# Kernel tuning notes

Hardware: AMD Instinct MI355X
Metric: run time of the kernel (lower is better)

Reference implementation:

```python
import jax, jax.numpy as jnp
import numpy as np

B, T, DIM = 2, 2048, 2048
H, DH = 16, 128
QC, KVC = 512, 512
DD = 64  # decoupled rope dim


def _rope_freqs(t, dd, theta=10000.0):
    inv = 1.0 / (theta ** (np.arange(0, dd, 2, dtype=np.float32) / dd))  # [dd/2]
    ang = np.arange(t, dtype=np.float32)[:, None] * inv[None, :]         # [T, dd/2]
    return jnp.asarray(np.stack([np.cos(ang), np.sin(ang)], axis=-1))    # [T, dd/2, 2]


def setup_inputs() -> dict:
    key = jax.random.key(0)
    ks = jax.random.split(key, 10)
    def w(k, i, o):
        return jax.random.normal(k, (i, o), jnp.float32) / np.sqrt(i)
    x = jax.random.normal(ks[0], (B, T, DIM), jnp.float32)
    freqs_cis = _rope_freqs(T, DD)
    neg = jnp.float32(-1e9)
    mask = jnp.where(jnp.tril(jnp.ones((T, T), bool)), 0.0, neg).astype(jnp.float32)
    return {
        "x": x, "freqs_cis": freqs_cis, "mask": mask,
        "W_dq": w(ks[1], DIM, QC), "W_uq": w(ks[2], QC, H * DH),
        "W_dkv": w(ks[3], DIM, KVC), "W_uk": w(ks[4], KVC, H * DH),
        "W_uv": w(ks[5], KVC, H * DH), "W_qr": w(ks[6], QC, H * DD),
        "W_kr": w(ks[7], DIM, DD), "W_o": w(ks[8], H * DH, DIM),
    }


def _apply_rope(t, freqs_cis):
    # t: [B, T, H, DD]; freqs_cis: [T, DD/2, 2]
    tp = t.reshape(*t.shape[:-1], -1, 2)               # [B,T,H,DD/2,2]
    cos = freqs_cis[None, :, None, :, 0]
    sin = freqs_cis[None, :, None, :, 1]
    x1, x2 = tp[..., 0], tp[..., 1]
    rot = jnp.stack([x1 * cos - x2 * sin, x1 * sin + x2 * cos], axis=-1)
    return rot.reshape(t.shape)


def reference(x, freqs_cis, mask, W_dq, W_uq, W_dkv, W_uk, W_uv, W_qr, W_kr, W_o):
    q_c = x @ W_dq                                     # [B,T,QC]
    kv_c = x @ W_dkv                                   # [B,T,KVC]
    q_rope = (q_c @ W_qr).reshape(B, T, H, DD)
    kv_rope = jnp.broadcast_to((x @ W_kr)[:, :, None, :], (B, T, H, DD))
    q_rope = _apply_rope(q_rope, freqs_cis)
    kv_rope = _apply_rope(kv_rope, freqs_cis)
    q = (q_c @ W_uq).reshape(B, T, H, DH)
    k = (kv_c @ W_uk).reshape(B, T, H, DH)
    v = (kv_c @ W_uv).reshape(B, T, H, DH)
    q = jnp.concatenate([q, q_rope], axis=-1)          # [B,T,H,DH+DD]
    k = jnp.concatenate([k, kv_rope], axis=-1)
    scale = 1.0 / np.sqrt(DH + DD)
    scores = jnp.einsum("bqhd,bkhd->bhqk", q, k) * scale + mask[None, None]
    attn = jax.nn.softmax(scores, axis=-1)
    out = jnp.einsum("bhqk,bkhd->bqhd", attn, v).reshape(B, T, H * DH)
    return out @ W_o
```

## Files before the change

### kernel.cpp

```cpp
#include <hip/hip_runtime.h>
#include <hip/hip_bf16.h>
#include <cstdint>
#include <cstddef>

typedef __bf16 bf16_t;
typedef __attribute__((ext_vector_type(8))) __bf16 bf16x8;
typedef __attribute__((ext_vector_type(4))) __bf16 bf16x4;
typedef __attribute__((ext_vector_type(4))) float f32x4;

#define B_ 2
#define T_ 2048
#define DIM_ 2048
#define H_ 16
#define DH_ 128
#define DD_ 64
#define DQK_ 192
#define QSTRIDE_ 3072
#define BT_ 4096

__device__ __forceinline__ void gload16(const void* g, void* lds) {
  __builtin_amdgcn_global_load_lds(
      (const __attribute__((address_space(1))) unsigned int*)g,
      (__attribute__((address_space(3))) unsigned int*)lds, 16, 0, 0);
}

struct bf16_4 { bf16_t a, b, c, d; };
__global__ void cast_f32_bf16(const float* __restrict__ in, bf16_t* __restrict__ out, int n4) {
  int i = blockIdx.x * blockDim.x + threadIdx.x;
  if (i >= n4) return;
  float4 v = ((const float4*)in)[i];
  bf16_4 r{(bf16_t)v.x, (bf16_t)v.y, (bf16_t)v.z, (bf16_t)v.w};
  ((bf16_4*)out)[i] = r;
}

__global__ void transpose_cast(const float* __restrict__ W, bf16_t* __restrict__ Wt,
                               int K, int N, int Np) {
  __shared__ float tile[32][33];
  int k0 = blockIdx.x * 32, n0 = blockIdx.y * 32;
  int tx = threadIdx.x, ty = threadIdx.y;
#pragma unroll
  for (int i = 0; i < 4; ++i) {
    int k = k0 + ty + i * 8, n = n0 + tx;
    float v = (k < K && n < N) ? W[(size_t)k * N + n] : 0.f;
    tile[ty + i * 8][tx] = v;
  }
  __syncthreads();
#pragma unroll
  for (int i = 0; i < 4; ++i) {
    int n = n0 + ty + i * 8, k = k0 + tx;
    if (n < Np && k < K) Wt[(size_t)n * K + k] = (bf16_t)tile[tx][ty + i * 8];
  }
}

__global__ void transpose_v(const bf16_t* __restrict__ V, bf16_t* __restrict__ Vt) {
  __shared__ bf16_t tile[64 * 64];
  int id = blockIdx.x;
  int t0 = (id & 31) * 64;
  int d0 = ((id >> 5) & 1) * 64;
  int bh = id >> 6;
  int b = bh >> 4, h = bh & 15;
  int t = threadIdx.x;
#pragma unroll
  for (int it = 0; it < 2; ++it) {
    int idx = it * 256 + t;
    int tt = idx >> 3, c = idx & 7;
    bf16x8 v = *(const bf16x8*)&V[(size_t)(b * T_ + t0 + tt) * 2048 + h * 128 + d0 + c * 8];
    int sw = (tt ^ (tt >> 3)) & 7;
    *(bf16x8*)((char*)tile + tt * 128 + 16 * (c ^ sw)) = v;
  }
  __syncthreads();
#pragma unroll
  for (int it = 0; it < 2; ++it) {
    int idx = it * 256 + t;
    int dr = idx >> 3, c = idx & 7;
    bf16_t tmp[8];
#pragma unroll
    for (int u = 0; u < 8; ++u) {
      int sw = (u ^ c) & 7;
      tmp[u] = *(const bf16_t*)((const char*)tile + (8 * c + u) * 128 + ((2 * dr) ^ (16 * sw)));
    }
    *(bf16x8*)&Vt[((size_t)bh * 128 + d0 + dr) * T_ + t0 + c * 8] = *(bf16x8*)tmp;
  }
}

template <int MODE>
__global__ __launch_bounds__(256) void gemm_bt(const bf16_t* __restrict__ A,
                                               const bf16_t* __restrict__ Bt,
                                               void* __restrict__ C0v,
                                               void* __restrict__ C1v,
                                               void* __restrict__ C2v,
                                               int M, int N, int K, int ldc) {
  __shared__ bf16_t As[128 * 32];
  __shared__ bf16_t Bs[128 * 32];
  const int t = threadIdx.x;
  const int w = t >> 6, l = t & 63, l15 = l & 15, lhi = l >> 4;
  const int m0 = blockIdx.y * 128, n0 = blockIdx.x * 128;
  const int wr = (w >> 1) * 64, wc = (w & 1) * 64;

  f32x4 zero = {0.f, 0.f, 0.f, 0.f};
  f32x4 acc[4][4];
#pragma unroll
  for (int m = 0; m < 4; ++m)
#pragma unroll
    for (int n = 0; n < 4; ++n) acc[m][n] = zero;

  const int e0 = t * 8;
  const int r0 = e0 >> 5, c0 = e0 & 31;
  const int e1 = 2048 + t * 8;
  const int r1 = e1 >> 5, c1 = e1 & 31;

  for (int k0 = 0; k0 < K; k0 += 32) {
    gload16(A + (size_t)(m0 + r0) * K + k0 + c0, &As[e0]);
    gload16(A + (size_t)(m0 + r1) * K + k0 + c1, &As[e1]);
    gload16(Bt + (size_t)(n0 + r0) * K + k0 + c0, &Bs[e0]);
    gload16(Bt + (size_t)(n0 + r1) * K + k0 + c1, &Bs[e1]);
    __syncthreads();
    bf16x8 af[4], bfr[4];
#pragma unroll
    for (int m = 0; m < 4; ++m)
      af[m] = *(const bf16x8*)&As[(wr + m * 16 + l15) * 32 + lhi * 8];
#pragma unroll
    for (int n = 0; n < 4; ++n)
      bfr[n] = *(const bf16x8*)&Bs[(wc + n * 16 + l15) * 32 + lhi * 8];
#pragma unroll
    for (int m = 0; m < 4; ++m)
#pragma unroll
      for (int n = 0; n < 4; ++n)
        acc[m][n] = __builtin_amdgcn_mfma_f32_16x16x32_bf16(af[m], bfr[n], acc[m][n], 0, 0, 0);
    __syncthreads();
  }

#pragma unroll
  for (int m = 0; m < 4; ++m) {
#pragma unroll
    for (int n = 0; n < 4; ++n) {
#pragma unroll
      for (int r = 0; r < 4; ++r) {
        int row = m0 + wr + m * 16 + lhi * 4 + r;
        int col = n0 + wc + n * 16 + l15;
        float v = acc[m][n][r];
        if (MODE == 1) {
          ((float*)C0v)[(size_t)row * ldc + col] = v;
        } else if (MODE == 3) {
          if (col < 512)       ((bf16_t*)C0v)[(size_t)row * 512 + col] = (bf16_t)v;
          else if (col < 1024) ((bf16_t*)C1v)[(size_t)row * 512 + (col - 512)] = (bf16_t)v;
          else if (col < 1088) ((bf16_t*)C2v)[(size_t)row * 64 + (col - 1024)] = (bf16_t)v;
        } else if (MODE == 4) {
          if (col < 2048) ((bf16_t*)C0v)[(size_t)row * QSTRIDE_ + (col >> 7) * DQK_ + (col & 127)] = (bf16_t)v;
          else            ((bf16_t*)C1v)[(size_t)row * 1024 + (col - 2048)] = (bf16_t)v;
        } else if (MODE == 5) {
          if (col < 2048) ((bf16_t*)C0v)[(size_t)row * QSTRIDE_ + (col >> 7) * DQK_ + (col & 127)] = (bf16_t)v;
          else            ((bf16_t*)C1v)[(size_t)row * 2048 + (col - 2048)] = (bf16_t)v;
        }
      }
    }
  }
}

__global__ void rope_q(const bf16_t* __restrict__ qr, const float* __restrict__ fr,
                       bf16_t* __restrict__ Q) {
  int idx = blockIdx.x * 256 + threadIdx.x;
  int j = idx & 31;
  int h = (idx >> 5) & 15;
  int row = idx >> 9;
  int tt = row & (T_ - 1);
  float x1 = (float)qr[(size_t)row * 1024 + h * 64 + 2 * j];
  float x2 = (float)qr[(size_t)row * 1024 + h * 64 + 2 * j + 1];
  float c = fr[tt * 64 + 2 * j], s = fr[tt * 64 + 2 * j + 1];
  bf16_t o0 = (bf16_t)(x1 * c - x2 * s);
  bf16_t o1 = (bf16_t)(x1 * s + x2 * c);
  size_t o = (size_t)row * QSTRIDE_ + h * DQK_ + 128 + 2 * j;
  Q[o] = o0;
  Q[o + 1] = o1;
}

__global__ void rope_k(const bf16_t* __restrict__ kr, const float* __restrict__ fr,
                       bf16_t* __restrict__ Kb) {
  int idx = blockIdx.x * 256 + threadIdx.x;
  int j = idx & 31;
  int row = idx >> 5;
  int tt = row & (T_ - 1);
  float x1 = (float)kr[(size_t)row * 64 + 2 * j];
  float x2 = (float)kr[(size_t)row * 64 + 2 * j + 1];
  float c = fr[tt * 64 + 2 * j], s = fr[tt * 64 + 2 * j + 1];
  union { bf16_t h2[2]; unsigned u; } pk;
  pk.h2[0] = (bf16_t)(x1 * c - x2 * s);
  pk.h2[1] = (bf16_t)(x1 * s + x2 * c);
#pragma unroll
  for (int h = 0; h < H_; ++h) {
    *(unsigned*)&Kb[(size_t)row * QSTRIDE_ + h * DQK_ + 128 + 2 * j] = pk.u;
  }
}

#define KLDB 200
#define VLDB 72
#define PLDB 68

__global__ __launch_bounds__(256, 2) void flash_attn3(const bf16_t* __restrict__ Q,
                                                      const bf16_t* __restrict__ Kb,
                                                      const bf16_t* __restrict__ Vt,
                                                      bf16_t* __restrict__ Ob) {
  __shared__ bf16_t Ks[64 * KLDB];
  __shared__ bf16_t Vs[128 * VLDB];
  __shared__ bf16_t Ps[4][16 * PLDB];

  const int t = threadIdx.x, w = t >> 6, l = t & 63, l15 = l & 15, lhi = l >> 4;
  const int id = blockIdx.x;
  const int xcd = id & 7, sub = id >> 3;
  const int bh = xcd * 4 + (sub >> 4);
  const int qp = sub & 15;
  const int b = bh >> 4, h = bh & 15;
  const int qa = qp, qb = 31 - qp;
  const float scale = 0.07216878364870322f;

  int rK[6], cK[6];
#pragma unroll
  for (int i = 0; i < 6; ++i) { int idx = i * 256 + t; rK[i] = idx / 24; cK[i] = idx % 24; }
  const int rVt = t >> 3, cV = t & 7;
  const bf16_t* kbase = Kb + (size_t)b * T_ * QSTRIDE_ + h * DQK_;
  const bf16_t* vbase = Vt + (size_t)bh * DH_ * T_;

  bf16x8 kreg[6], vreg[4];
#define LOAD_TILE(K0)                                                                      \
  do {                                                                                     \
    _Pragma("unroll") for (int i = 0; i < 6; ++i)                                          \
        kreg[i] = *(const bf16x8*)(kbase + (size_t)((K0) + rK[i]) * QSTRIDE_ + cK[i] * 8); \
    _Pragma("unroll") for (int i = 0; i < 4; ++i)                                          \
        vreg[i] = *(const bf16x8*)(vbase + (size_t)(i * 32 + rVt) * T_ + (K0) + cV * 8);   \
  } while (0)
#define WRITE_TILE()                                                                       \
  do {                                                                                     \
    _Pragma("unroll") for (int i = 0; i < 6; ++i)                                          \
        *(bf16x8*)&Ks[rK[i] * KLDB + cK[i] * 8] = kreg[i];                                 \
    _Pragma("unroll") for (int i = 0; i < 4; ++i)                                          \
        *(bf16x8*)&Vs[(i * 32 + rVt) * VLDB + cV * 8] = vreg[i];                           \
  } while (0)

  f32x4 zero = {0.f, 0.f, 0.f, 0.f};

  LOAD_TILE(0);
  WRITE_TILE();
  __syncthreads();

  for (int pass = 0; pass < 2; ++pass) {
    const int qt = pass ? qb : qa;

    bf16x8 qf[6];
    {
      const bf16_t* qrow = Q + ((size_t)(b * T_ + qt * 64 + w * 16 + l15)) * QSTRIDE_ + h * DQK_;
#pragma unroll
      for (int kc = 0; kc < 6; ++kc) qf[kc] = *(const bf16x8*)(qrow + kc * 32 + lhi * 8);
    }

    float m_r[4], l_r[4];
    f32x4 accO[8];
#pragma unroll
    for (int r = 0; r < 4; ++r) { m_r[r] = -1e30f; l_r[r] = 0.f; }
#pragma unroll
    for (int n = 0; n < 8; ++n) accO[n] = zero;

    for (int kt = 0; kt <= qt; ++kt) {
      const bool last = (kt == qt);
      const bool haveNext = !(pass == 1 && last);
      if (haveNext) LOAD_TILE(last ? 0 : (kt + 1) * 64);

      f32x4 s[4];
#pragma unroll
      for (int n = 0; n < 4; ++n) s[n] = zero;
      __builtin_amdgcn_s_setprio(1);
#pragma unroll
      for (int kc = 0; kc < 6; ++kc) {
#pragma unroll
        for (int n = 0; n < 4; ++n) {
          bf16x8 kf = *(const bf16x8*)&Ks[(n * 16 + l15) * KLDB + kc * 32 + lhi * 8];
          s[n] = __builtin_amdgcn_mfma_f32_16x16x32_bf16(qf[kc], kf, s[n], 0, 0, 0);
        }
      }
      __builtin_amdgcn_s_setprio(0);

#pragma unroll
      for (int n = 0; n < 4; ++n)
#pragma unroll
        for (int r = 0; r < 4; ++r) {
          float v = s[n][r] * scale;
          if (last) {
            int qq = w * 16 + lhi * 4 + r;
            int kk = n * 16 + l15;
            if (kk > qq) v = -1e30f;
          }
          s[n][r] = v;
        }
      float mn[4], corr[4];
#pragma unroll
      for (int r = 0; r < 4; ++r) {
        float v = fmaxf(fmaxf(s[0][r], s[1][r]), fmaxf(s[2][r], s[3][r]));
#pragma unroll
        for (int off = 1; off < 16; off <<= 1) v = fmaxf(v, __shfl_xor(v, off, 64));
        mn[r] = fmaxf(m_r[r], v);
        corr[r] = __expf(m_r[r] - mn[r]);
        m_r[r] = mn[r];
      }
      float rs[4] = {0.f, 0.f, 0.f, 0.f};
#pragma unroll
      for (int n = 0; n < 4; ++n)
#pragma unroll
        for (int r = 0; r < 4; ++r) {
          float p = __expf(s[n][r] - mn[r]);
          rs[r] += p;
          Ps[w][(lhi * 4 + r) * PLDB + n * 16 + l15] = (bf16_t)p;
        }
#pragma unroll
      for (int r = 0; r < 4; ++r) {
        float v = rs[r];
#pragma unroll
        for (int off = 1; off < 16; off <<= 1) v += __shfl_xor(v, off, 64);
        l_r[r] = l_r[r] * corr[r] + v;
      }
#pragma unroll
      for (int n = 0; n < 8; ++n)
#pragma unroll
        for (int r = 0; r < 4; ++r) accO[n][r] *= corr[r];

      __builtin_amdgcn_s_setprio(1);
#pragma unroll
      for (int kc = 0; kc < 2; ++kc) {
        bf16x4 p0 = *(const bf16x4*)&Ps[w][l15 * PLDB + kc * 32 + lhi * 8];
        bf16x4 p1 = *(const bf16x4*)&Ps[w][l15 * PLDB + kc * 32 + lhi * 8 + 4];
        bf16x8 pf = __builtin_shufflevector(p0, p1, 0, 1, 2, 3, 4, 5, 6, 7);
#pragma unroll
        for (int n = 0; n < 8; ++n) {
          bf16x8 vf = *(const bf16x8*)&Vs[(n * 16 + l15) * VLDB + kc * 32 + lhi * 8];
          accO[n] = __builtin_amdgcn_mfma_f32_16x16x32_bf16(pf, vf, accO[n], 0, 0, 0);
        }
      }
      __builtin_amdgcn_s_setprio(0);

      __syncthreads();
      if (haveNext) WRITE_TILE();
      __syncthreads();
    }

    {
      float inv[4];
#pragma unroll
      for (int r = 0; r < 4; ++r) inv[r] = 1.0f / l_r[r];
#pragma unroll
      for (int n = 0; n < 8; ++n)
#pragma unroll
        for (int r = 0; r < 4; ++r) {
          size_t row = (size_t)(b * T_ + qt * 64 + w * 16 + lhi * 4 + r);
          Ob[row * (H_ * DH_) + h * DH_ + n * 16 + l15] = (bf16_t)(accO[n][r] * inv[r]);
        }
    }
  }
#undef LOAD_TILE
#undef WRITE_TILE
}

extern "C" void kernel_launch(void* const* d_in, const int* in_sizes, int n_in,
                              void* d_out, int out_size, void* d_ws, size_t ws_size,
                              hipStream_t stream) {
  (void)in_sizes; (void)n_in; (void)out_size; (void)ws_size;
  const float* x    = (const float*)d_in[0];
  const float* fr   = (const float*)d_in[1];
  const float* Wdq  = (const float*)d_in[3];
  const float* Wuq  = (const float*)d_in[4];
  const float* Wdkv = (const float*)d_in[5];
  const float* Wuk  = (const float*)d_in[6];
  const float* Wuv  = (const float*)d_in[7];
  const float* Wqr  = (const float*)d_in[8];
  const float* Wkr  = (const float*)d_in[9];
  const float* Wo   = (const float*)d_in[10];
  float* out = (float*)d_out;

  char* ws = (char*)d_ws;
  size_t off = 0;
  auto alloc = [&](size_t bytes) -> void* {
    void* p = ws + off;
    off += (bytes + 255) & ~(size_t)255;
    return p;
  };
  bf16_t* x_bf   = (bf16_t*)alloc((size_t)BT_ * DIM_ * 2);
  bf16_t* Bt1    = (bf16_t*)alloc((size_t)1152 * 2048 * 2);
  bf16_t* Bt2    = (bf16_t*)alloc((size_t)3072 * 512 * 2);
  bf16_t* Bt3    = (bf16_t*)alloc((size_t)4096 * 512 * 2);
  bf16_t* Wo_t   = (bf16_t*)alloc((size_t)2048 * 2048 * 2);
  bf16_t* q_c    = (bf16_t*)alloc((size_t)BT_ * 512 * 2);
  bf16_t* kv_c   = (bf16_t*)alloc((size_t)BT_ * 512 * 2);
  bf16_t* q_rb   = (bf16_t*)alloc((size_t)BT_ * 1024 * 2);
  bf16_t* k_rb   = (bf16_t*)alloc((size_t)BT_ * 64 * 2);
  bf16_t* Qbuf   = (bf16_t*)alloc((size_t)BT_ * QSTRIDE_ * 2);
  bf16_t* Kbuf   = (bf16_t*)alloc((size_t)BT_ * QSTRIDE_ * 2);
  bf16_t* Vbuf   = (bf16_t*)alloc((size_t)BT_ * 2048 * 2);
  bf16_t* Vt_g   = (bf16_t*)alloc((size_t)BT_ * 2048 * 2);
  bf16_t* AObuf  = (bf16_t*)alloc((size_t)BT_ * 2048 * 2);

  dim3 tb(32, 8);
  cast_f32_bf16<<<(BT_ * DIM_ / 4 + 255) / 256, 256, 0, stream>>>(x, x_bf, BT_ * DIM_ / 4);
  transpose_cast<<<dim3(64, 16), tb, 0, stream>>>(Wdq,  Bt1,                        2048, 512, 512);
  transpose_cast<<<dim3(64, 16), tb, 0, stream>>>(Wdkv, Bt1 + (size_t)512 * 2048,   2048, 512, 512);
  transpose_cast<<<dim3(64, 4),  tb, 0, stream>>>(Wkr,  Bt1 + (size_t)1024 * 2048,  2048, 64, 128);
  transpose_cast<<<dim3(16, 64), tb, 0, stream>>>(Wuq,  Bt2,                        512, 2048, 2048);
  transpose_cast<<<dim3(16, 32), tb, 0, stream>>>(Wqr,  Bt2 + (size_t)2048 * 512,   512, 1024, 1024);
  transpose_cast<<<dim3(16, 64), tb, 0, stream>>>(Wuk,  Bt3,                        512, 2048, 2048);
  transpose_cast<<<dim3(16, 64), tb, 0, stream>>>(Wuv,  Bt3 + (size_t)2048 * 512,   512, 2048, 2048);
  transpose_cast<<<dim3(64, 64), tb, 0, stream>>>(Wo,   Wo_t,                       2048, 2048, 2048);

  gemm_bt<3><<<dim3(9, 32),  256, 0, stream>>>(x_bf, Bt1, q_c, kv_c, k_rb, BT_, 1088, 2048, 0);
  gemm_bt<4><<<dim3(24, 32), 256, 0, stream>>>(q_c,  Bt2, Qbuf, q_rb, nullptr, BT_, 3072, 512, 0);
  gemm_bt<5><<<dim3(32, 32), 256, 0, stream>>>(kv_c, Bt3, Kbuf, Vbuf, nullptr, BT_, 4096, 512, 0);

  transpose_v<<<2048, 256, 0, stream>>>(Vbuf, Vt_g);

  rope_q<<<(BT_ * H_ * 32) / 256, 256, 0, stream>>>(q_rb, fr, Qbuf);
  rope_k<<<(BT_ * 32) / 256, 256, 0, stream>>>(k_rb, fr, Kbuf);

  flash_attn3<<<512, 256, 0, stream>>>(Qbuf, Kbuf, Vt_g, AObuf);

  gemm_bt<1><<<dim3(16, 32), 256, 0, stream>>>(AObuf, Wo_t, out, nullptr, nullptr, BT_, 2048, 2048, 2048);
}
```

Before: 324.3 us.

## Rewrite flash attention with 128-row Q tiles, double-buffered async LDS loads and swizzle

The attention kernel now handles 128 query rows per block, with each wave owning 32 rows across two MFMA sub-tiles that share each K/V fragment read from LDS. K/V tiles are staged with direct global-to-LDS loads into double buffers using an XOR swizzle instead of padded rows, and the second barrier per step is removed. Grid shrinks to 256 blocks with one block per CU and causal pairing across 16 tiles. The intent is better reuse of LDS data and overlap of loads with compute. The cost is fewer waves for latency hiding, and waves on the diagonal tiles idle while others finish.

```diff
diff --git a/kernel.cpp b/kernel.cpp
--- a/kernel.cpp
+++ b/kernel.cpp
@@ -192,169 +192,200 @@
   }
 }
 
-#define KLDB 200
-#define VLDB 72
+#define KSLOT 24
+#define KBYTES (64 * KSLOT * 16)
+#define VSLOT 8
+#define VBYTES (128 * VSLOT * 16)
 #define PLDB 68
-
-__global__ __launch_bounds__(256, 2) void flash_attn3(const bf16_t* __restrict__ Q,
+#define PSBYTES (4 * 32 * PLDB * 2)
+#define SMEM_TOTAL (2 * KBYTES + 2 * VBYTES + PSBYTES)
+
+__global__ __launch_bounds__(256, 1) void flash_attn4(const bf16_t* __restrict__ Q,
                                                       const bf16_t* __restrict__ Kb,
                                                       const bf16_t* __restrict__ Vt,
                                                       bf16_t* __restrict__ Ob) {
-  __shared__ bf16_t Ks[64 * KLDB];
-  __shared__ bf16_t Vs[128 * VLDB];
-  __shared__ bf16_t Ps[4][16 * PLDB];
+  extern __shared__ char smem[];
+  char* ksmem = smem;
+  char* vsmem = smem + 2 * KBYTES;
+  bf16_t* Ps = (bf16_t*)(smem + 2 * KBYTES + 2 * VBYTES);
 
   const int t = threadIdx.x, w = t >> 6, l = t & 63, l15 = l & 15, lhi = l >> 4;
   const int id = blockIdx.x;
-  const int xcd = id & 7, sub = id >> 3;
-  const int bh = xcd * 4 + (sub >> 4);
-  const int qp = sub & 15;
+  const int bh = id & 31, qp = id >> 5;
   const int b = bh >> 4, h = bh & 15;
-  const int qa = qp, qb = 31 - qp;
+  const int qa = qp, qb = 15 - qp;
   const float scale = 0.07216878364870322f;
 
-  int rK[6], cK[6];
-#pragma unroll
-  for (int i = 0; i < 6; ++i) { int idx = i * 256 + t; rK[i] = idx / 24; cK[i] = idx % 24; }
-  const int rVt = t >> 3, cV = t & 7;
   const bf16_t* kbase = Kb + (size_t)b * T_ * QSTRIDE_ + h * DQK_;
   const bf16_t* vbase = Vt + (size_t)bh * DH_ * T_;
 
-  bf16x8 kreg[6], vreg[4];
-#define LOAD_TILE(K0)                                                                      \
-  do {                                                                                     \
-    _Pragma("unroll") for (int i = 0; i < 6; ++i)                                          \
-        kreg[i] = *(const bf16x8*)(kbase + (size_t)((K0) + rK[i]) * QSTRIDE_ + cK[i] * 8); \
-    _Pragma("unroll") for (int i = 0; i < 4; ++i)                                          \
-        vreg[i] = *(const bf16x8*)(vbase + (size_t)(i * 32 + rVt) * T_ + (K0) + cV * 8);   \
-  } while (0)
-#define WRITE_TILE()                                                                       \
-  do {                                                                                     \
-    _Pragma("unroll") for (int i = 0; i < 6; ++i)                                          \
-        *(bf16x8*)&Ks[rK[i] * KLDB + cK[i] * 8] = kreg[i];                                 \
-    _Pragma("unroll") for (int i = 0; i < 4; ++i)                                          \
-        *(bf16x8*)&Vs[(i * 32 + rVt) * VLDB + cV * 8] = vreg[i];                           \
-  } while (0)
+  int koff[6];
+#pragma unroll
+  for (int j = 0; j < 6; ++j) {
+    int i = j * 256 + t;
+    int r = i / 24, p = i % 24;
+    int s = (p & ~7) | ((p & 7) ^ (r & 7));
+    koff[j] = r * QSTRIDE_ + s * 8;
+  }
+  int voff[4];
+#pragma unroll
+  for (int j = 0; j < 4; ++j) {
+    int i = j * 256 + t;
+    int r = i >> 3, p = i & 7;
+    int s = p ^ (r & 7);
+    voff[j] = r * T_ + s * 8;
+  }
+  const int xk = l15 & 7;
+
+  auto STAGE = [&](int buf, int k0) {
+    const bf16_t* kg = kbase + (size_t)k0 * QSTRIDE_;
+    char* kd = ksmem + buf * KBYTES + w * 1024;
+#pragma unroll
+    for (int j = 0; j < 6; ++j) gload16(kg + koff[j], kd + j * 4096);
+    const bf16_t* vg = vbase + k0;
+    char* vd = vsmem + buf * VBYTES + w * 1024;
+#pragma unroll
+    for (int j = 0; j < 4; ++j) gload16(vg + voff[j], vd + j * 4096);
+  };
 
   f32x4 zero = {0.f, 0.f, 0.f, 0.f};
-
-  LOAD_TILE(0);
-  WRITE_TILE();
-  __syncthreads();
+  int cur = 0;
+  STAGE(0, 0);
 
   for (int pass = 0; pass < 2; ++pass) {
-    const int qt = pass ? qb : qa;
-
-    bf16x8 qf[6];
-    {
-      const bf16_t* qrow = Q + ((size_t)(b * T_ + qt * 64 + w * 16 + l15)) * QSTRIDE_ + h * DQK_;
-#pragma unroll
-      for (int kc = 0; kc < 6; ++kc) qf[kc] = *(const bf16x8*)(qrow + kc * 32 + lhi * 8);
-    }
-
-    float m_r[4], l_r[4];
-    f32x4 accO[8];
-#pragma unroll
-    for (int r = 0; r < 4; ++r) { m_r[r] = -1e30f; l_r[r] = 0.f; }
-#pragma unroll
-    for (int n = 0; n < 8; ++n) accO[n] = zero;
-
-    for (int kt = 0; kt <= qt; ++kt) {
-      const bool last = (kt == qt);
-      const bool haveNext = !(pass == 1 && last);
-      if (haveNext) LOAD_TILE(last ? 0 : (kt + 1) * 64);
-
-      f32x4 s[4];
-#pragma unroll
-      for (int n = 0; n < 4; ++n) s[n] = zero;
-      __builtin_amdgcn_s_setprio(1);
-#pragma unroll
-      for (int kc = 0; kc < 6; ++kc) {
-#pragma unroll
-        for (int n = 0; n < 4; ++n) {
-          bf16x8 kf = *(const bf16x8*)&Ks[(n * 16 + l15) * KLDB + kc * 32 + lhi * 8];
-          s[n] = __builtin_amdgcn_mfma_f32_16x16x32_bf16(qf[kc], kf, s[n], 0, 0, 0);
+    const int q = pass ? qb : qa;
+    const int nkt = 2 * q + 2;
+    const int myLast = 2 * q + (w >= 2 ? 1 : 0);
+
+    bf16x8 qf[2][6];
+#pragma unroll
+    for (int u = 0; u < 2; ++u) {
+      const bf16_t* qrow = Q + ((size_t)(b * T_ + q * 128 + w * 32 + u * 16 + l15)) * QSTRIDE_ + h * DQK_;
+#pragma unroll
+      for (int kc = 0; kc < 6; ++kc) qf[u][kc] = *(const bf16x8*)(qrow + kc * 32 + lhi * 8);
+    }
+
+    float m_r[2][4], l_r[2][4];
+    f32x4 accO[2][8];
+#pragma unroll
+    for (int u = 0; u < 2; ++u) {
+#pragma unroll
+      for (int r = 0; r < 4; ++r) { m_r[u][r] = -1e30f; l_r[u][r] = 0.f; }
+#pragma unroll
+      for (int n = 0; n < 8; ++n) accO[u][n] = zero;
+    }
+
+    for (int kt = 0; kt < nkt; ++kt) {
+      const bool lastStep = (pass == 1) && (kt == nkt - 1);
+      if (!lastStep) STAGE(cur ^ 1, (kt == nkt - 1) ? 0 : (kt + 1) * 64);
+
+      if (kt <= myLast) {
+        const char* ks = ksmem + cur * KBYTES;
+        const char* vs = vsmem + cur * VBYTES;
+        const bool diag = (kt == myLast);
+
+        f32x4 s[2][4];
+#pragma unroll
+        for (int u = 0; u < 2; ++u)
+#pragma unroll
+          for (int n = 0; n < 4; ++n) s[u][n] = zero;
+#pragma unroll
+        for (int kc = 0; kc < 6; ++kc) {
+          const int sl = 4 * kc + lhi;
+          const int p = (sl & ~7) | ((sl & 7) ^ xk);
+#pragma unroll
+          for (int n = 0; n < 4; ++n) {
+            bf16x8 kf = *(const bf16x8*)(ks + ((n * 16 + l15) * KSLOT + p) * 16);
+            s[0][n] = __builtin_amdgcn_mfma_f32_16x16x32_bf16(qf[0][kc], kf, s[0][n], 0, 0, 0);
+            s[1][n] = __builtin_amdgcn_mfma_f32_16x16x32_bf16(qf[1][kc], kf, s[1][n], 0, 0, 0);
+          }
+        }
+
+#pragma unroll
+        for (int u = 0; u < 2; ++u) {
+#pragma unroll
+          for (int n = 0; n < 4; ++n)
+#pragma unroll
+            for (int r = 0; r < 4; ++r) {
+              float v = s[u][n][r] * scale;
+              if (diag) {
+                int qq = (w & 1) * 32 + u * 16 + lhi * 4 + r;
+                int kk = n * 16 + l15;
+                if (kk > qq) v = -1e30f;
+              }
+              s[u][n][r] = v;
+            }
+          float mn[4], corr[4];
+#pragma unroll
+          for (int r = 0; r < 4; ++r) {
+            float v = fmaxf(fmaxf(s[u][0][r], s[u][1][r]), fmaxf(s[u][2][r], s[u][3][r]));
+#pragma unroll
+            for (int off = 1; off < 16; off <<= 1) v = fmaxf(v, __shfl_xor(v, off, 64));
+            mn[r] = fmaxf(m_r[u][r], v);
+            corr[r] = __expf(m_r[u][r] - mn[r]);
+            m_r[u][r] = mn[r];
+          }
+          float rs[4] = {0.f, 0.f, 0.f, 0.f};
+#pragma unroll
+          for (int n = 0; n < 4; ++n)
+#pragma unroll
+            for (int r = 0; r < 4; ++r) {
+              float p = __expf(s[u][n][r] - mn[r]);
+              rs[r] += p;
+              Ps[(w * 32 + u * 16 + lhi * 4 + r) * PLDB + n * 16 + l15] = (bf16_t)p;
+            }
+#pragma unroll
+          for (int r = 0; r < 4; ++r) {
+            float v = rs[r];
+#pragma unroll
+            for (int off = 1; off < 16; off <<= 1) v += __shfl_xor(v, off, 64);
+            l_r[u][r] = l_r[u][r] * corr[r] + v;
+          }
+#pragma unroll
+          for (int n = 0; n < 8; ++n)
+#pragma unroll
+            for (int r = 0; r < 4; ++r) accO[u][n][r] *= corr[r];
+        }
+
+#pragma unroll
+        for (int kc = 0; kc < 2; ++kc) {
+          bf16x8 pfu[2];
+#pragma unroll
+          for (int u = 0; u < 2; ++u) {
+            const bf16_t* pb = Ps + (w * 32 + u * 16 + l15) * PLDB + kc * 32 + lhi * 8;
+            bf16x4 p0 = *(const bf16x4*)pb;
+            bf16x4 p1 = *(const bf16x4*)(pb + 4);
+            pfu[u] = __builtin_shufflevector(p0, p1, 0, 1, 2, 3, 4, 5, 6, 7);
+          }
+          const int sv = 4 * kc + lhi;
+          const int pv = sv ^ xk;
+#pragma unroll
+          for (int n = 0; n < 8; ++n) {
+            bf16x8 vf = *(const bf16x8*)(vs + ((n * 16 + l15) * VSLOT + pv) * 16);
+            accO[0][n] = __builtin_amdgcn_mfma_f32_16x16x32_bf16(pfu[0], vf, accO[0][n], 0, 0, 0);
+            accO[1][n] = __builtin_amdgcn_mfma_f32_16x16x32_bf16(pfu[1], vf, accO[1][n], 0, 0, 0);
+          }
         }
       }
-      __builtin_amdgcn_s_setprio(0);
-
-#pragma unroll
-      for (int n = 0; n < 4; ++n)
+
+      __syncthreads();
+      cur ^= 1;
+    }
+
+#pragma unroll
+    for (int u = 0; u < 2; ++u) {
+      float inv[4];
+#pragma unroll
+      for (int r = 0; r < 4; ++r) inv[r] = 1.0f / l_r[u][r];
+#pragma unroll
+      for (int n = 0; n < 8; ++n)
 #pragma unroll
         for (int r = 0; r < 4; ++r) {
-          float v = s[n][r] * scale;
-          if (last) {
-            int qq = w * 16 + lhi * 4 + r;
-            int kk = n * 16 + l15;
-            if (kk > qq) v = -1e30f;
-          }
-          s[n][r] = v;
+          size_t row = (size_t)(b * T_ + q * 128 + w * 32 + u * 16 + lhi * 4 + r);
+          Ob[row * (H_ * DH_) + h * DH_ + n * 16 + l15] = (bf16_t)(accO[u][n][r] * inv[r]);
         }
-      float mn[4], corr[4];
-#pragma unroll
-      for (int r = 0; r < 4; ++r) {
-        float v = fmaxf(fmaxf(s[0][r], s[1][r]), fmaxf(s[2][r], s[3][r]));
-#pragma unroll
-        for (int off = 1; off < 16; off <<= 1) v = fmaxf(v, __shfl_xor(v, off, 64));
-        mn[r] = fmaxf(m_r[r], v);
-        corr[r] = __expf(m_r[r] - mn[r]);
-        m_r[r] = mn[r];
-      }
-      float rs[4] = {0.f, 0.f, 0.f, 0.f};
-#pragma unroll
-      for (int n = 0; n < 4; ++n)
-#pragma unroll
-        for (int r = 0; r < 4; ++r) {
-          float p = __expf(s[n][r] - mn[r]);
-          rs[r] += p;
-          Ps[w][(lhi * 4 + r) * PLDB + n * 16 + l15] = (bf16_t)p;
-        }
-#pragma unroll
-      for (int r = 0; r < 4; ++r) {
-        float v = rs[r];
-#pragma unroll
-        for (int off = 1; off < 16; off <<= 1) v += __shfl_xor(v, off, 64);
-        l_r[r] = l_r[r] * corr[r] + v;
-      }
-#pragma unroll
-      for (int n = 0; n < 8; ++n)
-#pragma unroll
-        for (int r = 0; r < 4; ++r) accO[n][r] *= corr[r];
-
-      __builtin_amdgcn_s_setprio(1);
-#pragma unroll
-      for (int kc = 0; kc < 2; ++kc) {
-        bf16x4 p0 = *(const bf16x4*)&Ps[w][l15 * PLDB + kc * 32 + lhi * 8];
-        bf16x4 p1 = *(const bf16x4*)&Ps[w][l15 * PLDB + kc * 32 + lhi * 8 + 4];
-        bf16x8 pf = __builtin_shufflevector(p0, p1, 0, 1, 2, 3, 4, 5, 6, 7);
-#pragma unroll
-        for (int n = 0; n < 8; ++n) {
-          bf16x8 vf = *(const bf16x8*)&Vs[(n * 16 + l15) * VLDB + kc * 32 + lhi * 8];
-          accO[n] = __builtin_amdgcn_mfma_f32_16x16x32_bf16(pf, vf, accO[n], 0, 0, 0);
-        }
-      }
-      __builtin_amdgcn_s_setprio(0);
-
-      __syncthreads();
-      if (haveNext) WRITE_TILE();
-      __syncthreads();
-    }
-
-    {
-      float inv[4];
-#pragma unroll
-      for (int r = 0; r < 4; ++r) inv[r] = 1.0f / l_r[r];
-#pragma unroll
-      for (int n = 0; n < 8; ++n)
-#pragma unroll
-        for (int r = 0; r < 4; ++r) {
-          size_t row = (size_t)(b * T_ + qt * 64 + w * 16 + lhi * 4 + r);
-          Ob[row * (H_ * DH_) + h * DH_ + n * 16 + l15] = (bf16_t)(accO[n][r] * inv[r]);
-        }
-    }
-  }
-#undef LOAD_TILE
-#undef WRITE_TILE
+    }
+  }
 }
 
 extern "C" void kernel_launch(void* const* d_in, const int* in_sizes, int n_in,
@@ -415,7 +446,9 @@
   rope_q<<<(BT_ * H_ * 32) / 256, 256, 0, stream>>>(q_rb, fr, Qbuf);
   rope_k<<<(BT_ * 32) / 256, 256, 0, stream>>>(k_rb, fr, Kbuf);
 
-  flash_attn3<<<512, 256, 0, stream>>>(Qbuf, Kbuf, Vt_g, AObuf);
+  hipFuncSetAttribute((const void*)flash_attn4,
+                      hipFuncAttributeMaxDynamicSharedMemorySize, SMEM_TOTAL);
+  flash_attn4<<<256, 256, SMEM_TOTAL, stream>>>(Qbuf, Kbuf, Vt_g, AObuf);
 
   gemm_bt<1><<<dim3(16, 32), 256, 0, stream>>>(AObuf, Wo_t, out, nullptr, nullptr, BT_, 2048, 2048, 2048);
 }
```

Result: slower. 378.9 us (+16.8%).

## Process both causal query tiles concurrently across warps sharing one K/V stream

Applied to the files above, without the earlier changes.

Each block used to handle its paired query tiles (qp and 31-qp) in two sequential passes, streaming K/V tiles twice. Now warps 0-1 own the short tile and warps 2-3 the long tile. Each warp computes 32 query rows, two 16-row MFMA groups, so each K/V fragment read from LDS is reused twice and a single pass over K/V serves both tiles. The block-to-work mapping also changes: head index now varies fastest and the second half of the grid reverses qp order. The cost is more registers per warp and idle warps 0-1 once the short tile finishes, which causes load imbalance inside the block.

```diff
diff --git a/kernel.cpp b/kernel.cpp
--- a/kernel.cpp
+++ b/kernel.cpp
@@ -196,21 +196,23 @@
 #define VLDB 72
 #define PLDB 68
 
-__global__ __launch_bounds__(256, 2) void flash_attn3(const bf16_t* __restrict__ Q,
+__global__ __launch_bounds__(256, 2) void flash_attn5(const bf16_t* __restrict__ Q,
                                                       const bf16_t* __restrict__ Kb,
                                                       const bf16_t* __restrict__ Vt,
                                                       bf16_t* __restrict__ Ob) {
   __shared__ bf16_t Ks[64 * KLDB];
   __shared__ bf16_t Vs[128 * VLDB];
-  __shared__ bf16_t Ps[4][16 * PLDB];
+  __shared__ bf16_t Ps[4][32 * PLDB];
 
   const int t = threadIdx.x, w = t >> 6, l = t & 63, l15 = l & 15, lhi = l >> 4;
   const int id = blockIdx.x;
-  const int xcd = id & 7, sub = id >> 3;
-  const int bh = xcd * 4 + (sub >> 4);
-  const int qp = sub & 15;
+  int bh, qp;
+  if (id < 256) { bh = id & 31; qp = id >> 5; }
+  else          { int j = id - 256; bh = j & 31; qp = 15 - (j >> 5); }
   const int b = bh >> 4, h = bh & 15;
   const int qa = qp, qb = 31 - qp;
+  const int q_s = (w >= 2) ? qb : qa;
+  const int wrow = (w & 1) * 32;
   const float scale = 0.07216878364870322f;
 
   int rK[6], cK[6];
@@ -238,120 +240,136 @@
 
   f32x4 zero = {0.f, 0.f, 0.f, 0.f};
 
+  bf16x8 qf[2][6];
+#pragma unroll
+  for (int u = 0; u < 2; ++u) {
+    const bf16_t* qrow =
+        Q + ((size_t)(b * T_ + q_s * 64 + wrow + u * 16 + l15)) * QSTRIDE_ + h * DQK_;
+#pragma unroll
+    for (int kc = 0; kc < 6; ++kc) qf[u][kc] = *(const bf16x8*)(qrow + kc * 32 + lhi * 8);
+  }
+
+  float m_r[2][4], l_r[2][4];
+  f32x4 accO[2][8];
+#pragma unroll
+  for (int u = 0; u < 2; ++u) {
+#pragma unroll
+    for (int r = 0; r < 4; ++r) { m_r[u][r] = -1e30f; l_r[u][r] = 0.f; }
+#pragma unroll
+    for (int n = 0; n < 8; ++n) accO[u][n] = zero;
+  }
+
   LOAD_TILE(0);
   WRITE_TILE();
   __syncthreads();
 
-  for (int pass = 0; pass < 2; ++pass) {
-    const int qt = pass ? qb : qa;
-
-    bf16x8 qf[6];
-    {
-      const bf16_t* qrow = Q + ((size_t)(b * T_ + qt * 64 + w * 16 + l15)) * QSTRIDE_ + h * DQK_;
-#pragma unroll
-      for (int kc = 0; kc < 6; ++kc) qf[kc] = *(const bf16x8*)(qrow + kc * 32 + lhi * 8);
-    }
-
-    float m_r[4], l_r[4];
-    f32x4 accO[8];
-#pragma unroll
-    for (int r = 0; r < 4; ++r) { m_r[r] = -1e30f; l_r[r] = 0.f; }
-#pragma unroll
-    for (int n = 0; n < 8; ++n) accO[n] = zero;
-
-    for (int kt = 0; kt <= qt; ++kt) {
-      const bool last = (kt == qt);
-      const bool haveNext = !(pass == 1 && last);
-      if (haveNext) LOAD_TILE(last ? 0 : (kt + 1) * 64);
-
-      f32x4 s[4];
-#pragma unroll
-      for (int n = 0; n < 4; ++n) s[n] = zero;
+  for (int kt = 0; kt <= qb; ++kt) {
+    if (kt < qb) LOAD_TILE((kt + 1) * 64);
+
+    if (kt <= q_s) {
+      const bool diag = (kt == q_s);
+
+      f32x4 s[2][4];
+#pragma unroll
+      for (int u = 0; u < 2; ++u)
+#pragma unroll
+        for (int n = 0; n < 4; ++n) s[u][n] = zero;
       __builtin_amdgcn_s_setprio(1);
 #pragma unroll
       for (int kc = 0; kc < 6; ++kc) {
 #pragma unroll
         for (int n = 0; n < 4; ++n) {
           bf16x8 kf = *(const bf16x8*)&Ks[(n * 16 + l15) * KLDB + kc * 32 + lhi * 8];
-          s[n] = __builtin_amdgcn_mfma_f32_16x16x32_bf16(qf[kc], kf, s[n], 0, 0, 0);
+          s[0][n] = __builtin_amdgcn_mfma_f32_16x16x32_bf16(qf[0][kc], kf, s[0][n], 0, 0, 0);
+          s[1][n] = __builtin_amdgcn_mfma_f32_16x16x32_bf16(qf[1][kc], kf, s[1][n], 0, 0, 0);
         }
       }
       __builtin_amdgcn_s_setprio(0);
 
 #pragma unroll
-      for (int n = 0; n < 4; ++n)
+      for (int u = 0; u < 2; ++u) {
+#pragma unroll
+        for (int n = 0; n < 4; ++n)
+#pragma unroll
+          for (int r = 0; r < 4; ++r) {
+            float v = s[u][n][r] * scale;
+            if (diag) {
+              int qq = wrow + u * 16 + lhi * 4 + r;
+              int kk = n * 16 + l15;
+              if (kk > qq) v = -1e30f;
+            }
+            s[u][n][r] = v;
+          }
+        float mn[4], corr[4];
 #pragma unroll
         for (int r = 0; r < 4; ++r) {
-          float v = s[n][r] * scale;
-          if (last) {
-            int qq = w * 16 + lhi * 4 + r;
-            int kk = n * 16 + l15;
-            if (kk > qq) v = -1e30f;
+          float v = fmaxf(fmaxf(s[u][0][r], s[u][1][r]), fmaxf(s[u][2][r], s[u][3][r]));
+#pragma unroll
+          for (int off = 1; off < 16; off <<= 1) v = fmaxf(v, __shfl_xor(v, off, 64));
+          mn[r] = fmaxf(m_r[u][r], v);
+          corr[r] = __expf(m_r[u][r] - mn[r]);
+          m_r[u][r] = mn[r];
+        }
+        float rs[4] = {0.f, 0.f, 0.f, 0.f};
+#pragma unroll
+        for (int n = 0; n < 4; ++n)
+#pragma unroll
+          for (int r = 0; r < 4; ++r) {
+            float p = __expf(s[u][n][r] - mn[r]);
+            rs[r] += p;
+            Ps[w][(u * 16 + lhi * 4 + r) * PLDB + n * 16 + l15] = (bf16_t)p;
           }
-          s[n][r] = v;
-        }
-      float mn[4], corr[4];
-#pragma unroll
-      for (int r = 0; r < 4; ++r) {
-        float v = fmaxf(fmaxf(s[0][r], s[1][r]), fmaxf(s[2][r], s[3][r]));
-#pragma unroll
-        for (int off = 1; off < 16; off <<= 1) v = fmaxf(v, __shfl_xor(v, off, 64));
-        mn[r] = fmaxf(m_r[r], v);
-        corr[r] = __expf(m_r[r] - mn[r]);
-        m_r[r] = mn[r];
+#pragma unroll
+        for (int r = 0; r < 4; ++r) {
+          float v = rs[r];
+#pragma unroll
+          for (int off = 1; off < 16; off <<= 1) v += __shfl_xor(v, off, 64);
+          l_r[u][r] = l_r[u][r] * corr[r] + v;
+        }
+#pragma unroll
+        for (int n = 0; n < 8; ++n)
+#pragma unroll
+          for (int r = 0; r < 4; ++r) accO[u][n][r] *= corr[r];
       }
-      float rs[4] = {0.f, 0.f, 0.f, 0.f};
-#pragma unroll
-      for (int n = 0; n < 4; ++n)
-#pragma unroll
-        for (int r = 0; r < 4; ++r) {
-          float p = __expf(s[n][r] - mn[r]);
-          rs[r] += p;
-          Ps[w][(lhi * 4 + r) * PLDB + n * 16 + l15] = (bf16_t)p;
-        }
-#pragma unroll
-      for (int r = 0; r < 4; ++r) {
-        float v = rs[r];
-#pragma unroll
-        for (int off = 1; off < 16; off <<= 1) v += __shfl_xor(v, off, 64);
-        l_r[r] = l_r[r] * corr[r] + v;
-      }
-#pragma unroll
-      for (int n = 0; n < 8; ++n)
-#pragma unroll
-        for (int r = 0; r < 4; ++r) accO[n][r] *= corr[r];
 
       __builtin_amdgcn_s_setprio(1);
 #pragma unroll
       for (int kc = 0; kc < 2; ++kc) {
-        bf16x4 p0 = *(const bf16x4*)&Ps[w][l15 * PLDB + kc * 32 + lhi * 8];
-        bf16x4 p1 = *(const bf16x4*)&Ps[w][l15 * PLDB + kc * 32 + lhi * 8 + 4];
-        bf16x8 pf = __builtin_shufflevector(p0, p1, 0, 1, 2, 3, 4, 5, 6, 7);
+        bf16x8 pf[2];
+#pragma unroll
+        for (int u = 0; u < 2; ++u) {
+          const bf16_t* pb = &Ps[w][(u * 16 + l15) * PLDB + kc * 32 + lhi * 8];
+          bf16x4 p0 = *(const bf16x4*)pb;
+          bf16x4 p1 = *(const bf16x4*)(pb + 4);
+          pf[u] = __builtin_shufflevector(p0, p1, 0, 1, 2, 3, 4, 5, 6, 7);
+        }
 #pragma unroll
         for (int n = 0; n < 8; ++n) {
           bf16x8 vf = *(const bf16x8*)&Vs[(n * 16 + l15) * VLDB + kc * 32 + lhi * 8];
-          accO[n] = __builtin_amdgcn_mfma_f32_16x16x32_bf16(pf, vf, accO[n], 0, 0, 0);
+          accO[0][n] = __builtin_amdgcn_mfma_f32_16x16x32_bf16(pf[0], vf, accO[0][n], 0, 0, 0);
+          accO[1][n] = __builtin_amdgcn_mfma_f32_16x16x32_bf16(pf[1], vf, accO[1][n], 0, 0, 0);
         }
       }
       __builtin_amdgcn_s_setprio(0);
-
-      __syncthreads();
-      if (haveNext) WRITE_TILE();
-      __syncthreads();
     }
 
-    {
-      float inv[4];
-#pragma unroll
-      for (int r = 0; r < 4; ++r) inv[r] = 1.0f / l_r[r];
-#pragma unroll
-      for (int n = 0; n < 8; ++n)
-#pragma unroll
-        for (int r = 0; r < 4; ++r) {
-          size_t row = (size_t)(b * T_ + qt * 64 + w * 16 + lhi * 4 + r);
-          Ob[row * (H_ * DH_) + h * DH_ + n * 16 + l15] = (bf16_t)(accO[n][r] * inv[r]);
-        }
-    }
+    __syncthreads();
+    if (kt < qb) WRITE_TILE();
+    __syncthreads();
+  }
+
+#pragma unroll
+  for (int u = 0; u < 2; ++u) {
+    float inv[4];
+#pragma unroll
+    for (int r = 0; r < 4; ++r) inv[r] = 1.0f / l_r[u][r];
+#pragma unroll
+    for (int n = 0; n < 8; ++n)
+#pragma unroll
+      for (int r = 0; r < 4; ++r) {
+        size_t row = (size_t)(b * T_ + q_s * 64 + wrow + u * 16 + lhi * 4 + r);
+        Ob[row * (H_ * DH_) + h * DH_ + n * 16 + l15] = (bf16_t)(accO[u][n][r] * inv[r]);
+      }
   }
 #undef LOAD_TILE
 #undef WRITE_TILE
@@ -415,7 +433,7 @@
   rope_q<<<(BT_ * H_ * 32) / 256, 256, 0, stream>>>(q_rb, fr, Qbuf);
   rope_k<<<(BT_ * 32) / 256, 256, 0, stream>>>(k_rb, fr, Kbuf);
 
-  flash_attn3<<<512, 256, 0, stream>>>(Qbuf, Kbuf, Vt_g, AObuf);
+  flash_attn5<<<512, 256, 0, stream>>>(Qbuf, Kbuf, Vt_g, AObuf);
 
   gemm_bt<1><<<dim3(16, 32), 256, 0, stream>>>(AObuf, Wo_t, out, nullptr, nullptr, BT_, 2048, 2048, 2048);
 }
```

After: 347.1 us. 7.0% more time.

## Fuse Q rope into up-projection GEMM epilogue and merge weight transposes

Applied to the files above, without the earlier changes.

Applies the rotary embedding to the q_rope columns directly in the GEMM epilogue, using a lane shuffle to fetch the paired element, and writes straight into the Q buffer. This removes the intermediate q_rb buffer and the separate rope_q kernel. It also folds eight weight transpose-cast launches into one kernel that dispatches on block index. Together these cut launch overhead and a global memory round trip, at the cost of extra epilogue work in the GEMM.

```diff
diff --git a/kernel.cpp b/kernel.cpp
--- a/kernel.cpp
+++ b/kernel.cpp
@@ -33,10 +33,24 @@
   ((bf16_4*)out)[i] = r;
 }
 
-__global__ void transpose_cast(const float* __restrict__ W, bf16_t* __restrict__ Wt,
-                               int K, int N, int Np) {
+__global__ void transpose_all(const float* __restrict__ Wdq, const float* __restrict__ Wdkv,
+                              const float* __restrict__ Wkr, const float* __restrict__ Wuq,
+                              const float* __restrict__ Wqr, const float* __restrict__ Wuk,
+                              const float* __restrict__ Wuv, const float* __restrict__ Wo,
+                              bf16_t* __restrict__ Bt1, bf16_t* __restrict__ Bt2,
+                              bf16_t* __restrict__ Bt3, bf16_t* __restrict__ Wo_t) {
   __shared__ float tile[32][33];
-  int k0 = blockIdx.x * 32, n0 = blockIdx.y * 32;
+  int id = blockIdx.x;
+  const float* W; bf16_t* Wt; int K, N, Np, kt;
+  if (id < 1024)      { W = Wdq;  Wt = Bt1;                          K = 2048; N = 512;  Np = 512;  kt = 64; }
+  else if (id < 2048) { W = Wdkv; Wt = Bt1 + (size_t)512 * 2048;  id -= 1024; K = 2048; N = 512;  Np = 512;  kt = 64; }
+  else if (id < 2304) { W = Wkr;  Wt = Bt1 + (size_t)1024 * 2048; id -= 2048; K = 2048; N = 64;   Np = 128;  kt = 64; }
+  else if (id < 3328) { W = Wuq;  Wt = Bt2;                       id -= 2304; K = 512;  N = 2048; Np = 2048; kt = 16; }
+  else if (id < 3840) { W = Wqr;  Wt = Bt2 + (size_t)2048 * 512;  id -= 3328; K = 512;  N = 1024; Np = 1024; kt = 16; }
+  else if (id < 4864) { W = Wuk;  Wt = Bt3;                       id -= 3840; K = 512;  N = 2048; Np = 2048; kt = 16; }
+  else if (id < 5888) { W = Wuv;  Wt = Bt3 + (size_t)2048 * 512;  id -= 4864; K = 512;  N = 2048; Np = 2048; kt = 16; }
+  else                { W = Wo;   Wt = Wo_t;                      id -= 5888; K = 2048; N = 2048; Np = 2048; kt = 64; }
+  int k0 = (id % kt) * 32, n0 = (id / kt) * 32;
   int tx = threadIdx.x, ty = threadIdx.y;
 #pragma unroll
   for (int i = 0; i < 4; ++i) {
@@ -89,6 +103,7 @@
                                                void* __restrict__ C0v,
                                                void* __restrict__ C1v,
                                                void* __restrict__ C2v,
+                                               const float* __restrict__ fr,
                                                int M, int N, int K, int ldc) {
   __shared__ bf16_t As[128 * 32];
   __shared__ bf16_t Bs[128 * 32];
@@ -146,8 +161,17 @@
           else if (col < 1024) ((bf16_t*)C1v)[(size_t)row * 512 + (col - 512)] = (bf16_t)v;
           else if (col < 1088) ((bf16_t*)C2v)[(size_t)row * 64 + (col - 1024)] = (bf16_t)v;
         } else if (MODE == 4) {
-          if (col < 2048) ((bf16_t*)C0v)[(size_t)row * QSTRIDE_ + (col >> 7) * DQK_ + (col & 127)] = (bf16_t)v;
-          else            ((bf16_t*)C1v)[(size_t)row * 1024 + (col - 2048)] = (bf16_t)v;
+          if (col < 2048) {
+            ((bf16_t*)C0v)[(size_t)row * QSTRIDE_ + (col >> 7) * DQK_ + (col & 127)] = (bf16_t)v;
+          } else {
+            float other = __shfl_xor(v, 1, 64);
+            int tt = row & (T_ - 1);
+            int j = (col & 63) >> 1;
+            float2 cs = ((const float2*)fr)[tt * 32 + j];
+            float o = (col & 1) ? (other * cs.y + v * cs.x) : (v * cs.x - other * cs.y);
+            int hh = (col - 2048) >> 6;
+            ((bf16_t*)C0v)[(size_t)row * QSTRIDE_ + hh * DQK_ + 128 + (col & 63)] = (bf16_t)o;
+          }
         } else if (MODE == 5) {
           if (col < 2048) ((bf16_t*)C0v)[(size_t)row * QSTRIDE_ + (col >> 7) * DQK_ + (col & 127)] = (bf16_t)v;
           else            ((bf16_t*)C1v)[(size_t)row * 2048 + (col - 2048)] = (bf16_t)v;
@@ -155,23 +179,6 @@
       }
     }
   }
-}
-
-__global__ void rope_q(const bf16_t* __restrict__ qr, const float* __restrict__ fr,
-                       bf16_t* __restrict__ Q) {
-  int idx = blockIdx.x * 256 + threadIdx.x;
-  int j = idx & 31;
-  int h = (idx >> 5) & 15;
-  int row = idx >> 9;
-  int tt = row & (T_ - 1);
-  float x1 = (float)qr[(size_t)row * 1024 + h * 64 + 2 * j];
-  float x2 = (float)qr[(size_t)row * 1024 + h * 64 + 2 * j + 1];
-  float c = fr[tt * 64 + 2 * j], s = fr[tt * 64 + 2 * j + 1];
-  bf16_t o0 = (bf16_t)(x1 * c - x2 * s);
-  bf16_t o1 = (bf16_t)(x1 * s + x2 * c);
-  size_t o = (size_t)row * QSTRIDE_ + h * DQK_ + 128 + 2 * j;
-  Q[o] = o0;
-  Q[o + 1] = o1;
 }
 
 __global__ void rope_k(const bf16_t* __restrict__ kr, const float* __restrict__ fr,
@@ -387,7 +394,6 @@
   bf16_t* Wo_t   = (bf16_t*)alloc((size_t)2048 * 2048 * 2);
   bf16_t* q_c    = (bf16_t*)alloc((size_t)BT_ * 512 * 2);
   bf16_t* kv_c   = (bf16_t*)alloc((size_t)BT_ * 512 * 2);
-  bf16_t* q_rb   = (bf16_t*)alloc((size_t)BT_ * 1024 * 2);
   bf16_t* k_rb   = (bf16_t*)alloc((size_t)BT_ * 64 * 2);
   bf16_t* Qbuf   = (bf16_t*)alloc((size_t)BT_ * QSTRIDE_ * 2);
   bf16_t* Kbuf   = (bf16_t*)alloc((size_t)BT_ * QSTRIDE_ * 2);
@@ -395,27 +401,18 @@
   bf16_t* Vt_g   = (bf16_t*)alloc((size_t)BT_ * 2048 * 2);
   bf16_t* AObuf  = (bf16_t*)alloc((size_t)BT_ * 2048 * 2);
 
-  dim3 tb(32, 8);
   cast_f32_bf16<<<(BT_ * DIM_ / 4 + 255) / 256, 256, 0, stream>>>(x, x_bf, BT_ * DIM_ / 4);
-  transpose_cast<<<dim3(64, 16), tb, 0, stream>>>(Wdq,  Bt1,                        2048, 512, 512);
-  transpose_cast<<<dim3(64, 16), tb, 0, stream>>>(Wdkv, Bt1 + (size_t)512 * 2048,   2048, 512, 512);
-  transpose_cast<<<dim3(64, 4),  tb, 0, stream>>>(Wkr,  Bt1 + (size_t)1024 * 2048,  2048, 64, 128);
-  transpose_cast<<<dim3(16, 64), tb, 0, stream>>>(Wuq,  Bt2,                        512, 2048, 2048);
-  transpose_cast<<<dim3(16, 32), tb, 0, stream>>>(Wqr,  Bt2 + (size_t)2048 * 512,   512, 1024, 1024);
-  transpose_cast<<<dim3(16, 64), tb, 0, stream>>>(Wuk,  Bt3,                        512, 2048, 2048);
-  transpose_cast<<<dim3(16, 64), tb, 0, stream>>>(Wuv,  Bt3 + (size_t)2048 * 512,   512, 2048, 2048);
-  transpose_cast<<<dim3(64, 64), tb, 0, stream>>>(Wo,   Wo_t,                       2048, 2048, 2048);
-
-  gemm_bt<3><<<dim3(9, 32),  256, 0, stream>>>(x_bf, Bt1, q_c, kv_c, k_rb, BT_, 1088, 2048, 0);
-  gemm_bt<4><<<dim3(24, 32), 256, 0, stream>>>(q_c,  Bt2, Qbuf, q_rb, nullptr, BT_, 3072, 512, 0);
-  gemm_bt<5><<<dim3(32, 32), 256, 0, stream>>>(kv_c, Bt3, Kbuf, Vbuf, nullptr, BT_, 4096, 512, 0);
+  transpose_all<<<9984, dim3(32, 8), 0, stream>>>(Wdq, Wdkv, Wkr, Wuq, Wqr, Wuk, Wuv, Wo,
+                                                  Bt1, Bt2, Bt3, Wo_t);
+
+  gemm_bt<3><<<dim3(9, 32),  256, 0, stream>>>(x_bf, Bt1, q_c, kv_c, k_rb, nullptr, BT_, 1088, 2048, 0);
+  gemm_bt<4><<<dim3(24, 32), 256, 0, stream>>>(q_c,  Bt2, Qbuf, nullptr, nullptr, fr, BT_, 3072, 512, 0);
+  gemm_bt<5><<<dim3(32, 32), 256, 0, stream>>>(kv_c, Bt3, Kbuf, Vbuf, nullptr, nullptr, BT_, 4096, 512, 0);
 
   transpose_v<<<2048, 256, 0, stream>>>(Vbuf, Vt_g);
-
-  rope_q<<<(BT_ * H_ * 32) / 256, 256, 0, stream>>>(q_rb, fr, Qbuf);
   rope_k<<<(BT_ * 32) / 256, 256, 0, stream>>>(k_rb, fr, Kbuf);
 
   flash_attn3<<<512, 256, 0, stream>>>(Qbuf, Kbuf, Vt_g, AObuf);
 
-  gemm_bt<1><<<dim3(16, 32), 256, 0, stream>>>(AObuf, Wo_t, out, nullptr, nullptr, BT_, 2048, 2048, 2048);
-}
+  gemm_bt<1><<<dim3(16, 32), 256, 0, stream>>>(AObuf, Wo_t, out, nullptr, nullptr, nullptr, BT_, 2048, 2048, 2048);
+}
```

Result: no change. 318.7 us (-1.7%).
